# Kernel tuning notes

Hardware: AMD Instinct MI355X
Metric: run time of the kernel (lower is better)

Reference implementation:

```python
import jax, jax.numpy as jnp
import numpy as np

N, T, V, C, O = 64, 512, 17, 3, 64
EPS = 1e-5  # torch BatchNorm eps


def _bn(x, gamma, beta):
    # training-mode BatchNorm2d over (N, H, W) per channel, biased variance
    m = jnp.mean(x, axis=(0, 2, 3), keepdims=True)
    v = jnp.var(x, axis=(0, 2, 3), keepdims=True)
    return gamma.reshape(1, -1, 1, 1) * (x - m) * jax.lax.rsqrt(v + EPS) + beta.reshape(1, -1, 1, 1)


def setup_inputs() -> dict:
    key = jax.random.key(0)
    ks = jax.random.split(key, 20)
    f32 = jnp.float32
    PA = (jnp.eye(V, dtype=f32) / (1.0 + 1e-5))  # row-normalized identity, as in reset_parameter
    return {
        "x": jax.random.normal(ks[0], (N, T, V, C), f32),
        "w1": jax.random.normal(ks[1], (C, C), f32) * 0.5,
        "b1": jax.random.normal(ks[2], (C,), f32) * 0.1,
        "w2": jax.random.normal(ks[3], (C, C), f32) * 0.5,
        "b2": jax.random.normal(ks[4], (C,), f32) * 0.1,
        "convT_w": jax.random.normal(ks[5], (C,), f32) * 0.5,      # Conv2d(3,1,1) weight squeezed
        "convT_b": jax.random.normal(ks[6], (), f32) * 0.1,
        "convT_gamma": jnp.ones((), f32),
        "convT_beta": jnp.zeros((), f32),
        "PA": PA,
        "alpha": jnp.ones((V, V), f32),
        "conv2d_w": jax.random.normal(ks[7], (O, C), f32) * (2.0 / (O * 1 * 1)) ** 0.5,  # conv_branch_init
        "conv2d_b": jnp.zeros((O,), f32),
        "bn_gamma": jnp.full((O,), 1e-6, f32),  # bn_init(self.bn, 1e-6)
        "bn_beta": jnp.zeros((O,), f32),
        "pool_w": jax.random.normal(ks[8], (O, C), f32) * (2.0 / C) ** 0.5,  # kaiming fan_out-ish
        "pool_b": jnp.zeros((O,), f32),
        "pool_gamma": jnp.ones((O,), f32),
        "pool_beta": jnp.zeros((O,), f32),
    }


def reference(x, w1, b1, w2, b2, convT_w, convT_b, convT_gamma, convT_beta,
              PA, alpha, conv2d_w, conv2d_b, bn_gamma, bn_beta,
              pool_w, pool_b, pool_gamma, pool_beta):
    # x: (N, T, V, C)
    x1 = x @ w1.T + b1                     # linear1, (N,T,V,C)
    x2 = x @ w2.T + b2                     # linear2
    # d[n,t,i,j,c] = x1[n,t,j,c] - x2[n,t,i,c]; the 1x1 conv over C is linear,
    # so contract with convT_w BEFORE broadcasting to avoid the (N,T,V,V,C) tensor.
    a1 = x1 @ convT_w                      # (N,T,V)
    a2 = x2 @ convT_w                      # (N,T,V)
    s = a1[:, :, None, :] - a2[:, :, :, None] + convT_b   # (N,T,V,V)
    # BatchNorm2d(1): single channel -> stats over the whole tensor; then ReLU
    m = jnp.mean(s)
    var = jnp.var(s)
    s = jax.nn.relu(convT_gamma * (s - m) * jax.lax.rsqrt(var + EPS) + convT_beta)
    # temporal abs-diff, sum over T, mean over batch -> learned adjacency offset (V,V)
    a3 = jnp.mean(jnp.sum(jnp.abs(s[:, 1:] - s[:, :-1]), axis=1), axis=0)
    # NOTE: the original does x.view(N, C, T, V) -- a raw memory reinterpretation,
    # NOT a permute. Replicate with reshape.
    xr = x.reshape(N, C, T, V)
    A = PA + alpha * a3                    # (V,V)
    y = (xr.reshape(N, C * T, V) @ A).reshape(N, C, T, V)
    z = jnp.einsum('nctv,oc->notv', y, conv2d_w) + conv2d_b[None, :, None, None]
    z = _bn(z, bn_gamma, bn_beta)
    p = jnp.einsum('nctv,oc->notv', xr, pool_w) + pool_b[None, :, None, None]
    p = _bn(p, pool_gamma, pool_beta)
    out = jax.nn.relu(z + p)               # (N,O,T,V)
    return out.reshape(N, T, V, O)         # raw reshape, matching torch .reshape
```

## Files before the change

kernel.cpp:

```cpp
#include <hip/hip_runtime.h>

constexpr int Nn = 64, Tt = 512, Vv = 17, Oo = 64;
constexpr int TV  = Tt * Vv;
constexpr int CTV = 3 * TV;
constexpr float EPSf = 1e-5f;
constexpr int NG   = 51;
constexpr int GSTR = 2688;
constexpr int NGE  = 2652;
constexpr int BTV  = 1088;

__device__ inline int div17(int v) { return (int)(((unsigned)v * 61681u) >> 20); }

__device__ inline double wred(double v) {
#pragma unroll
  for (int o = 32; o > 0; o >>= 1) v += __shfl_down(v, o, 64);
  return v;
}

__global__ void __launch_bounds__(256) k1(
    const float* __restrict__ x,
    const float* __restrict__ w1, const float* __restrict__ b1,
    const float* __restrict__ w2, const float* __restrict__ b2,
    const float* __restrict__ cw, const float* __restrict__ cb,
    double* __restrict__ spart, float* __restrict__ gpart)
{
  __shared__ float wr[64 * 56];
  __shared__ float xsA[64 * 51];
  __shared__ double dred[4][5];
  const int tid = threadIdx.x, bid = blockIdx.x;
  const int n = bid >> 3, ch = bid & 7;

  {
    const float4* src = (const float4*)(x + (size_t)bid * 3264);
    float4* dst = (float4*)xsA;
    for (int i = tid; i < 816; i += 256) dst[i] = src[i];
  }
#pragma unroll
  for (int c = 0; c < 3; ++c) {
    const float4* src = (const float4*)(x + (size_t)n * CTV + (size_t)c * TV + ch * BTV);
    for (int i = tid; i < 272; i += 256) {
      float4 v = src[i];
      int p = i * 4;
      float vv[4] = { v.x, v.y, v.z, v.w };
#pragma unroll
      for (int k = 0; k < 4; ++k) {
        int pp = p + k; int t = div17(pp), u = pp - t * 17;
        wr[t * 56 + c * 17 + u] = vv[k];
      }
    }
  }
  for (int i = tid; i < 64 * 5; i += 256) { int t = i / 5, j = 51 + (i - t * 5); wr[t * 56 + j] = 0.f; }
  __syncthreads();

  float u1[3], u2[3];
#pragma unroll
  for (int k = 0; k < 3; ++k) {
    float s1 = 0.f, s2 = 0.f;
#pragma unroll
    for (int c = 0; c < 3; ++c) { s1 += cw[c] * w1[c * 3 + k]; s2 += cw[c] * w2[c * 3 + k]; }
    u1[k] = s1; u2[k] = s2;
  }
  float d1 = 0.f, d2 = 0.f;
#pragma unroll
  for (int c = 0; c < 3; ++c) { d1 += b1[c] * cw[c]; d2 += b2[c] * cw[c]; }
  const float bb = cb[0];

  if (tid < 49) {
    const int r8 = (tid / 7) * 8, c8 = (tid - (tid / 7) * 7) * 8;
    float acc[8][8];
#pragma unroll
    for (int a = 0; a < 8; ++a)
#pragma unroll
      for (int b = 0; b < 8; ++b) acc[a][b] = 0.f;
    for (int t = 0; t < 64; ++t) {
      const float* row = &wr[t * 56];
      float4 ra0 = *(const float4*)(row + r8), ra1 = *(const float4*)(row + r8 + 4);
      float4 cb0 = *(const float4*)(row + c8), cb1 = *(const float4*)(row + c8 + 4);
      float ae[8] = { ra0.x, ra0.y, ra0.z, ra0.w, ra1.x, ra1.y, ra1.z, ra1.w };
      float be[8] = { cb0.x, cb0.y, cb0.z, cb0.w, cb1.x, cb1.y, cb1.z, cb1.w };
#pragma unroll
      for (int a = 0; a < 8; ++a)
#pragma unroll
        for (int b = 0; b < 8; ++b) acc[a][b] = fmaf(ae[a], be[b], acc[a][b]);
    }
    float* gp = gpart + (size_t)bid * GSTR;
#pragma unroll
    for (int a = 0; a < 8; ++a) {
      int j = r8 + a;
      if (j < NG) {
#pragma unroll
        for (int b = 0; b < 8; ++b) {
          int jp = c8 + b;
          if (jp < NG) gp[j * NG + jp] = acc[a][b];
        }
      }
    }
  }

  double st[5] = {0, 0, 0, 0, 0};
  if (tid >= 64 && tid < 128) {
    const float* rp = &xsA[(tid - 64) * 51];
    float A = 0.f, G = 0.f, Q1 = 0.f, Q2 = 0.f;
#pragma unroll
    for (int v = 0; v < 17; ++v) {
      float x0 = rp[v * 3], x1 = rp[v * 3 + 1], x2 = rp[v * 3 + 2];
      float va1 = fmaf(x0, u1[0], fmaf(x1, u1[1], fmaf(x2, u1[2], d1)));
      float va2 = fmaf(x0, u2[0], fmaf(x1, u2[1], fmaf(x2, u2[2], d2)));
      float g = bb - va2;
      A += va1; G += g;
      Q1 = fmaf(va1, va1, Q1); Q2 = fmaf(g, g, Q2);
    }
    st[0] = A; st[1] = G; st[2] = Q1; st[3] = Q2; st[4] = (double)A * (double)G;
  }
  if (tid >= 128 && tid < 128 + NG) {
    int j = tid - 128;
    float m = 0.f;
    for (int t = 0; t < 64; ++t) m += wr[t * 56 + j];
    gpart[(size_t)bid * GSTR + NG * NG + j] = m;
  }

  {
    int wv = tid >> 6;
#pragma unroll
    for (int s = 0; s < 5; ++s) { double r = wred(st[s]); if ((tid & 63) == 0) dred[wv][s] = r; }
  }
  __syncthreads();
  if (tid < 5)
    spart[(size_t)bid * 5 + tid] = dred[0][tid] + dred[1][tid] + dred[2][tid] + dred[3][tid];
}

__global__ void __launch_bounds__(256) k2(
    const float* __restrict__ x, const double* __restrict__ spart,
    const float* __restrict__ gpart,
    const float* __restrict__ w1, const float* __restrict__ b1,
    const float* __restrict__ w2, const float* __restrict__ b2,
    const float* __restrict__ cw, const float* __restrict__ cb,
    const float* __restrict__ cg_, const float* __restrict__ cbeta,
    float* __restrict__ a3part, double* __restrict__ gramF)
{
  __shared__ float l1t[17 * 260];
  __shared__ float l2t[17 * 260];
  __shared__ float segsum[289 * 4];
  __shared__ double dred[4][21];
  __shared__ float sfl[2];
  const int tid = threadIdx.x;
  const int h = blockIdx.x, n = blockIdx.y;
  const int jb = n * 2 + h;
  const int t0 = h * 256;
  const int wv = tid >> 6;

  {
    double v5[5];
#pragma unroll
    for (int s = 0; s < 5; ++s)
      v5[s] = spart[(size_t)tid * 5 + s] + spart[(size_t)(tid + 256) * 5 + s];
#pragma unroll
    for (int s = 0; s < 5; ++s) { double r = wred(v5[s]); if ((tid & 63) == 0) dred[wv][s] = r; }
  }
  __syncthreads();
  if (tid == 0) {
    double S[5];
#pragma unroll
    for (int s = 0; s < 5; ++s) S[s] = dred[0][s] + dred[1][s] + dred[2][s] + dred[3][s];
    double cnt = (double)Nn * Tt * Vv * Vv;
    double mean = ((double)Vv * (S[0] + S[1])) / cnt;
    double m2   = ((double)Vv * (S[2] + S[3]) + 2.0 * S[4]) / cnt;
    double var  = m2 - mean * mean;
    double scale = (double)cg_[0] / sqrt(var + (double)EPSf);
    double shift = (double)cbeta[0] + scale * ((double)cb[0] - mean);
    sfl[0] = (float)scale; sfl[1] = (float)(shift - scale * (double)cb[0]);
  }
  __syncthreads();

  {
    int e0 = jb * 21;
    double gv[21];
    const float* g1 = gpart + (size_t)tid * GSTR + e0;
    const float* g2 = gpart + (size_t)(tid + 256) * GSTR + e0;
#pragma unroll
    for (int k = 0; k < 21; ++k) gv[k] = (double)g1[k] + (double)g2[k];
#pragma unroll
    for (int k = 0; k < 21; ++k) { double r = wred(gv[k]); if ((tid & 63) == 0) dred[wv][k] = r; }
    __syncthreads();
    if (tid < 21 && e0 + tid < NGE)
      gramF[e0 + tid] = dred[0][tid] + dred[1][tid] + dred[2][tid] + dred[3][tid];
  }

  float u1[3], u2[3];
#pragma unroll
  for (int k = 0; k < 3; ++k) {
    float s1 = 0.f, s2 = 0.f;
#pragma unroll
    for (int c = 0; c < 3; ++c) { s1 += cw[c] * w1[c * 3 + k]; s2 += cw[c] * w2[c * 3 + k]; }
    u1[k] = s1; u2[k] = s2;
  }
  float d1 = 0.f, d2 = 0.f;
#pragma unroll
  for (int c = 0; c < 3; ++c) { d1 += b1[c] * cw[c]; d2 += b2[c] * cw[c]; }
  const float bb = cb[0];

  const int nst = (h == 0) ? 257 : 256;
  const float* xb = x + ((size_t)(n * Tt + t0)) * 51;
  for (int idx = tid; idx < nst * 17; idx += 256) {
    int r = div17(idx), v = idx - r * 17;
    const float* xp = xb + idx * 3;
    float x0 = xp[0], x1 = xp[1], x2 = xp[2];
    float va1 = fmaf(x0, u1[0], fmaf(x1, u1[1], fmaf(x2, u1[2], d1)));
    float va2 = fmaf(x0, u2[0], fmaf(x1, u2[1], fmaf(x2, u2[2], d2)));
    l1t[v * 260 + r] = va1; l2t[v * 260 + r] = bb - va2;
  }
  __syncthreads();

  {
    const float scale = sfl[0], c0 = sfl[1];
    for (int task = tid; task < 289 * 4; task += 256) {
      int e = task >> 2, s = task & 3;
      int i = div17(e), j = e - i * 17;
      int ts = s * 64;
      bool hasb = !(h == 1 && s == 3);
      const float* J = &l1t[j * 260];
      const float* I = &l2t[i * 260];
      float prev = fmaxf(fmaf(scale, J[ts] + I[ts], c0), 0.f);
      float acc = 0.f;
#pragma unroll 4
      for (int q = 0; q < 16; ++q) {
        float4 a4 = *(const float4*)(J + ts + q * 4);
        float4 b4 = *(const float4*)(I + ts + q * 4);
        float z0 = fmaxf(fmaf(scale, a4.x + b4.x, c0), 0.f);
        float z1 = fmaxf(fmaf(scale, a4.y + b4.y, c0), 0.f);
        float z2 = fmaxf(fmaf(scale, a4.z + b4.z, c0), 0.f);
        float z3 = fmaxf(fmaf(scale, a4.w + b4.w, c0), 0.f);
        if (q > 0) acc += fabsf(z0 - prev);
        acc += fabsf(z1 - z0) + fabsf(z2 - z1) + fabsf(z3 - z2);
        prev = z3;
      }
      if (hasb) {
        float zb = fmaxf(fmaf(scale, J[ts + 64] + I[ts + 64], c0), 0.f);
        acc += fabsf(zb - prev);
      }
      segsum[e * 4 + s] = acc;
    }
  }
  __syncthreads();

  for (int e = tid; e < 289; e += 256) {
    float s = (segsum[e * 4] + segsum[e * 4 + 1]) + (segsum[e * 4 + 2] + segsum[e * 4 + 3]);
    a3part[(size_t)jb * 289 + e] = s;
  }
}

__global__ void __launch_bounds__(256, 2) k3(
    const float* __restrict__ x,
    const float* __restrict__ PA, const float* __restrict__ alpha,
    const float* __restrict__ a3part, const double* __restrict__ gramF,
    const float* __restrict__ c2w, const float* __restrict__ c2b,
    const float* __restrict__ bng, const float* __restrict__ bnb,
    const float* __restrict__ pw, const float* __restrict__ pb,
    const float* __restrict__ pg, const float* __restrict__ pbeta,
    float* __restrict__ out)
{
  __shared__ float xs[3 * BTV], ys[3 * BTV];
  __shared__ float As[289], Bh[289], rsA[17], coefs[512];
  __shared__ double gs[NGE];
  __shared__ double mom[18];
  const int tid = threadIdx.x, bid = blockIdx.x;
  const int n = bid >> 3, ch = bid & 7;
  const int t0c = ch * BTV;

#pragma unroll
  for (int c = 0; c < 3; ++c) {
    const float4* src = (const float4*)(x + (size_t)n * CTV + (size_t)c * TV + t0c);
    float4* dst = (float4*)(xs + c * BTV);
    for (int i = tid; i < 272; i += 256) dst[i] = src[i];
  }

  for (int e = tid; e < NGE; e += 256) gs[e] = gramF[e];
  for (int e = tid; e < 289; e += 256) {
    float acc = 0.f;
#pragma unroll 4
    for (int j = 0; j < 128; ++j) acc += a3part[(size_t)j * 289 + e];
    As[e] = fmaf(alpha[e], acc * (1.0f / Nn), PA[e]);
  }
  __syncthreads();

  for (int k = tid; k < 289; k += 256) {
    int u = div17(k), up = k - u * 17;
    float s = 0.f;
#pragma unroll
    for (int v = 0; v < 17; ++v) s = fmaf(As[u * 17 + v], As[up * 17 + v], s);
    Bh[k] = s;
  }
  if (tid < 17) {
    float s = 0.f;
#pragma unroll
    for (int v = 0; v < 17; ++v) s += As[tid * 17 + v];
    rsA[tid] = s;
  }
  __syncthreads();

  {
    const int pc0[6] = {0, 0, 0, 1, 1, 2};
    const int pc1[6] = {0, 1, 2, 1, 2, 2};
    if (tid < 192) {
      int p = tid >> 5, r = tid & 31;
      int c = pc0[p], cp = pc1[p];
      double s = 0.0;
      for (int k = r; k < 289; k += 32) {
        int u = div17(k), up = k - u * 17;
        s += gs[(c * 17 + u) * NG + cp * 17 + up] * (double)Bh[k];
      }
#pragma unroll
      for (int off = 16; off > 0; off >>= 1) s += __shfl_down(s, off, 32);
      if (r == 0) mom[3 + p] = s;
    } else if (tid < 198) {
      int p = tid - 192; int c = pc0[p], cp = pc1[p];
      double s = 0.0;
#pragma unroll
      for (int u = 0; u < 17; ++u) s += gs[(c * 17 + u) * NG + cp * 17 + u];
      mom[12 + p] = s;
    } else if (tid < 201) {
      int c = tid - 198; double s = 0.0;
#pragma unroll
      for (int u = 0; u < 17; ++u) s += gs[NG * NG + c * 17 + u] * (double)rsA[u];
      mom[c] = s;
    } else if (tid < 204) {
      int c = tid - 201; double s = 0.0;
#pragma unroll
      for (int u = 0; u < 17; ++u) s += gs[NG * NG + c * 17 + u];
      mom[9 + c] = s;
    }
  }
  __syncthreads();

  if (tid < 64) {
    int o = tid;
    const double cnt = (double)Nn * Tt * Vv;
    double my0 = mom[0] / cnt, my1 = mom[1] / cnt, my2 = mom[2] / cnt;
    double e00 = mom[3] / cnt, e01 = mom[4] / cnt, e02 = mom[5] / cnt;
    double e11 = mom[6] / cnt, e12 = mom[7] / cnt, e22 = mom[8] / cnt;
    double mx0 = mom[9] / cnt, mx1 = mom[10] / cnt, mx2 = mom[11] / cnt;
    double f00 = mom[12] / cnt, f01 = mom[13] / cnt, f02 = mom[14] / cnt;
    double f11 = mom[15] / cnt, f12 = mom[16] / cnt, f22 = mom[17] / cnt;
    double w0 = c2w[o * 3], w1_ = c2w[o * 3 + 1], w2_ = c2w[o * 3 + 2], bz = c2b[o];
    double wm = w0 * my0 + w1_ * my1 + w2_ * my2, mz = wm + bz;
    double Ez2 = w0 * w0 * e00 + 2 * w0 * w1_ * e01 + 2 * w0 * w2_ * e02
               + w1_ * w1_ * e11 + 2 * w1_ * w2_ * e12 + w2_ * w2_ * e22
               + 2 * bz * wm + bz * bz;
    double sz = (double)bng[o] / sqrt(Ez2 - mz * mz + (double)EPSf);
    double q0 = pw[o * 3], q1 = pw[o * 3 + 1], q2 = pw[o * 3 + 2], bp = pb[o];
    double qm = q0 * mx0 + q1 * mx1 + q2 * mx2, mp = qm + bp;
    double Ep2 = q0 * q0 * f00 + 2 * q0 * q1 * f01 + 2 * q0 * q2 * f02
               + q1 * q1 * f11 + 2 * q1 * q2 * f12 + q2 * q2 * f22
               + 2 * bp * qm + bp * bp;
    double sp = (double)pg[o] / sqrt(Ep2 - mp * mp + (double)EPSf);
    coefs[o * 8 + 0] = (float)(sz * w0); coefs[o * 8 + 1] = (float)(sz * w1_); coefs[o * 8 + 2] = (float)(sz * w2_);
    coefs[o * 8 + 3] = (float)(sp * q0); coefs[o * 8 + 4] = (float)(sp * q1); coefs[o * 8 + 5] = (float)(sp * q2);
    coefs[o * 8 + 6] = (float)(sz * (bz - mz) + (double)bnb[o] + sp * (bp - mp) + (double)pbeta[o]);
    coefs[o * 8 + 7] = 0.f;
  }
#pragma unroll
  for (int k = 0; k < 5; ++k) {
    int e = k * 256 + tid;
    if (e < BTV) {
      int tr = div17(e), v = e - tr * 17;
      float y0 = 0.f, y1 = 0.f, y2 = 0.f;
#pragma unroll
      for (int u = 0; u < 17; ++u) {
        float a = As[u * 17 + v];
        y0 = fmaf(xs[tr * 17 + u], a, y0);
        y1 = fmaf(xs[BTV + tr * 17 + u], a, y1);
        y2 = fmaf(xs[2 * BTV + tr * 17 + u], a, y2);
      }
      ys[e] = y0; ys[BTV + e] = y1; ys[2 * BTV + e] = y2;
    }
  }
  __syncthreads();

  float* ob = out + (size_t)n * ((size_t)Oo * TV) + t0c;
#pragma unroll 2
  for (int k = 0; k < 68; ++k) {
    int idx = k * 256 + tid;
    int o = div17(idx >> 4);
    int q = idx - o * 272, tq = q * 4;
    float4 y0 = *(const float4*)&ys[tq];
    float4 y1 = *(const float4*)&ys[BTV + tq];
    float4 y2 = *(const float4*)&ys[2 * BTV + tq];
    float4 x0 = *(const float4*)&xs[tq];
    float4 x1 = *(const float4*)&xs[BTV + tq];
    float4 x2 = *(const float4*)&xs[2 * BTV + tq];
    float a0 = coefs[o * 8 + 0], a1 = coefs[o * 8 + 1], a2 = coefs[o * 8 + 2];
    float p0 = coefs[o * 8 + 3], p1 = coefs[o * 8 + 4], p2 = coefs[o * 8 + 5];
    float be = coefs[o * 8 + 6];
    float4 r;
    r.x = fmaxf(fmaf(a0, y0.x, fmaf(a1, y1.x, fmaf(a2, y2.x, fmaf(p0, x0.x, fmaf(p1, x1.x, fmaf(p2, x2.x, be)))))), 0.f);
    r.y = fmaxf(fmaf(a0, y0.y, fmaf(a1, y1.y, fmaf(a2, y2.y, fmaf(p0, x0.y, fmaf(p1, x1.y, fmaf(p2, x2.y, be)))))), 0.f);
    r.z = fmaxf(fmaf(a0, y0.z, fmaf(a1, y1.z, fmaf(a2, y2.z, fmaf(p0, x0.z, fmaf(p1, x1.z, fmaf(p2, x2.z, be)))))), 0.f);
    r.w = fmaxf(fmaf(a0, y0.w, fmaf(a1, y1.w, fmaf(a2, y2.w, fmaf(p0, x0.w, fmaf(p1, x1.w, fmaf(p2, x2.w, be)))))), 0.f);
    *(float4*)(ob + (size_t)o * TV + tq) = r;
  }
}

extern "C" void kernel_launch(void* const* d_in, const int* in_sizes, int n_in,
                              void* d_out, int out_size, void* d_ws, size_t ws_size,
                              hipStream_t stream)
{
  (void)in_sizes; (void)n_in; (void)out_size; (void)ws_size;
  const float* x     = (const float*)d_in[0];
  const float* w1    = (const float*)d_in[1];
  const float* b1    = (const float*)d_in[2];
  const float* w2    = (const float*)d_in[3];
  const float* b2    = (const float*)d_in[4];
  const float* cw    = (const float*)d_in[5];
  const float* cb    = (const float*)d_in[6];
  const float* cg_   = (const float*)d_in[7];
  const float* cbeta = (const float*)d_in[8];
  const float* PA    = (const float*)d_in[9];
  const float* alpha = (const float*)d_in[10];
  const float* c2w   = (const float*)d_in[11];
  const float* c2b   = (const float*)d_in[12];
  const float* bng   = (const float*)d_in[13];
  const float* bnb   = (const float*)d_in[14];
  const float* pw    = (const float*)d_in[15];
  const float* pb    = (const float*)d_in[16];
  const float* pg    = (const float*)d_in[17];
  const float* pbeta = (const float*)d_in[18];
  float* out = (float*)d_out;

  char* ws = (char*)d_ws;
  double* spart  = (double*)(ws + 0);
  float*  gpart  = (float*)(ws + 20480);
  float*  a3part = (float*)(ws + 5525504);
  double* gramF  = (double*)(ws + 5673472);

  hipLaunchKernelGGL(k1, dim3(512), dim3(256), 0, stream,
                     x, w1, b1, w2, b2, cw, cb, spart, gpart);
  hipLaunchKernelGGL(k2, dim3(2, Nn), dim3(256), 0, stream,
                     x, spart, gpart, w1, b1, w2, b2, cw, cb, cg_, cbeta, a3part, gramF);
  hipLaunchKernelGGL(k3, dim3(512), dim3(256), 0, stream,
                     x, PA, alpha, a3part, gramF, c2w, c2b, bng, bnb,
                     pw, pb, pg, pbeta, out);
}
```

Before: 89.22 us.

## Fuse three kernels into one cooperative kernel with custom grid barriers

Replaces the three-kernel pipeline with a single cooperative kernel of 512 blocks that synchronises through a hand-written atomic grid barrier, keeping per-block data in LDS across phases. Global statistics and the adjacency offset are accumulated with fixed-point 64-bit atomics instead of partial-sum buffers and separate reduction passes, and the temporal-diff work is redistributed per block. The aim is to remove kernel launch gaps and re-reads of x between stages. The cost is barrier spin overhead, a small init kernel, and reliance on co-residency; the old three-kernel path is kept as a fallback.

```diff
diff --git a/kernel.cpp b/kernel.cpp
--- a/kernel.cpp
+++ b/kernel.cpp
@@ -4,10 +4,12 @@
 constexpr int TV  = Tt * Vv;
 constexpr int CTV = 3 * TV;
 constexpr float EPSf = 1e-5f;
+constexpr int NB   = 512;
 constexpr int NG   = 51;
 constexpr int GSTR = 2688;
 constexpr int NGE  = 2652;
 constexpr int BTV  = 1088;
+constexpr double FXS = 16777216.0;
 
 __device__ inline int div17(int v) { return (int)(((unsigned)v * 61681u) >> 20); }
 
@@ -17,7 +19,354 @@
   return v;
 }
 
-__global__ void __launch_bounds__(256) k1(
+__global__ void __launch_bounds__(256) kinit(int* __restrict__ barr, long long* __restrict__ acc) {
+  for (int i = threadIdx.x; i < 520; i += 256) barr[i] = 0;
+  for (int i = threadIdx.x; i < 304; i += 256) acc[i] = 0;
+}
+
+__device__ inline void gridbar(int* slots, int* gen, int bid, int marker) {
+  __syncthreads();
+  if (threadIdx.x == 0) {
+    __threadfence();
+    __hip_atomic_store(slots + bid, marker, __ATOMIC_RELEASE, __HIP_MEMORY_SCOPE_AGENT);
+  }
+  if (bid == 0) {
+    for (int i = threadIdx.x; i < NB; i += 256) {
+      while (__hip_atomic_load(slots + i, __ATOMIC_ACQUIRE, __HIP_MEMORY_SCOPE_AGENT) < marker)
+        __builtin_amdgcn_s_sleep(8);
+    }
+    __syncthreads();
+    if (threadIdx.x == 0)
+      __hip_atomic_store(gen, marker, __ATOMIC_RELEASE, __HIP_MEMORY_SCOPE_AGENT);
+  } else if (threadIdx.x == 0) {
+    while (__hip_atomic_load(gen, __ATOMIC_ACQUIRE, __HIP_MEMORY_SCOPE_AGENT) < marker)
+      __builtin_amdgcn_s_sleep(64);
+  }
+  __syncthreads();
+}
+
+__global__ void __launch_bounds__(256, 2) fused(
+    const float* __restrict__ x,
+    const float* __restrict__ w1, const float* __restrict__ b1,
+    const float* __restrict__ w2, const float* __restrict__ b2,
+    const float* __restrict__ cw, const float* __restrict__ cb,
+    const float* __restrict__ cg_, const float* __restrict__ cbeta,
+    const float* __restrict__ PA, const float* __restrict__ alpha,
+    const float* __restrict__ c2w, const float* __restrict__ c2b,
+    const float* __restrict__ bng, const float* __restrict__ bnb,
+    const float* __restrict__ pw, const float* __restrict__ pb,
+    const float* __restrict__ pg, const float* __restrict__ pbeta,
+    float* __restrict__ out,
+    int* __restrict__ barr, long long* __restrict__ accum,
+    float* __restrict__ gpart, double* __restrict__ gramF)
+{
+  __shared__ float smem[6528];
+  __shared__ float As[289], Bh[289], rsA[17], coefs[512];
+  __shared__ double dred[4][6];
+  __shared__ double mom[18];
+  __shared__ float sfl[2];
+  float* l1t = smem;
+  float* l2t = smem + 1173;
+  float* wr  = smem + 2346;
+  double* scrD = (double*)&smem[2348];
+  float* xs  = smem;
+  float* ys  = smem + 3264;
+  int* slots = barr;
+  int* gen   = barr + NB;
+  long long* sstats  = accum;
+  long long* a3fixed = accum + 8;
+
+  const int tid = threadIdx.x, bid = blockIdx.x;
+  const int n = bid >> 3, ch = bid & 7;
+  const int t0 = ch * 64;
+
+  float u1[3], u2[3];
+#pragma unroll
+  for (int k = 0; k < 3; ++k) {
+    float s1 = 0.f, s2 = 0.f;
+#pragma unroll
+    for (int c = 0; c < 3; ++c) { s1 += cw[c] * w1[c * 3 + k]; s2 += cw[c] * w2[c * 3 + k]; }
+    u1[k] = s1; u2[k] = s2;
+  }
+  float d1 = 0.f, d2 = 0.f;
+#pragma unroll
+  for (int c = 0; c < 3; ++c) { d1 += b1[c] * cw[c]; d2 += b2[c] * cw[c]; }
+  const float bb = cb[0];
+
+  {
+    const int nload = (ch == 7) ? 64 : 65;
+    for (int idx = tid; idx < nload * 17; idx += 256) {
+      int r = div17(idx), v = idx - r * 17;
+      const float* xp = x + ((size_t)((n * Tt + t0 + r) * 17 + v)) * 3;
+      float x0 = xp[0], x1 = xp[1], x2 = xp[2];
+      float va1 = fmaf(x0, u1[0], fmaf(x1, u1[1], fmaf(x2, u1[2], d1)));
+      float va2 = fmaf(x0, u2[0], fmaf(x1, u2[1], fmaf(x2, u2[2], d2)));
+      l1t[v * 69 + r] = va1; l2t[v * 69 + r] = bb - va2;
+    }
+#pragma unroll
+    for (int c = 0; c < 3; ++c) {
+      const float4* src = (const float4*)(x + (size_t)n * CTV + (size_t)c * TV + ch * BTV);
+      for (int i = tid; i < 272; i += 256) {
+        float4 v = src[i];
+        int p = i * 4;
+        float vv[4] = { v.x, v.y, v.z, v.w };
+#pragma unroll
+        for (int k = 0; k < 4; ++k) {
+          int pp = p + k; int t = div17(pp), u = pp - t * 17;
+          wr[t * 56 + c * 17 + u] = vv[k];
+        }
+      }
+    }
+    for (int i = tid; i < 64 * 5; i += 256) { int t = i / 5, j = 51 + (i - t * 5); wr[t * 56 + j] = 0.f; }
+    __syncthreads();
+
+    if (tid < 64) {
+      float sA = 0.f, sG = 0.f, Q1 = 0.f, Q2 = 0.f;
+#pragma unroll
+      for (int v = 0; v < 17; ++v) {
+        float a = l1t[v * 69 + tid], g = l2t[v * 69 + tid];
+        sA += a; sG += g;
+        Q1 = fmaf(a, a, Q1); Q2 = fmaf(g, g, Q2);
+      }
+      double st[5] = { (double)sA, (double)sG, (double)Q1, (double)Q2,
+                       (double)sA * (double)sG };
+#pragma unroll
+      for (int s = 0; s < 5; ++s) {
+        double r = wred(st[s]);
+        if (tid == 0)
+          atomicAdd((unsigned long long*)&sstats[s], (unsigned long long)(long long)llrint(r * FXS));
+      }
+    }
+    if (tid < 49) {
+      const int r8 = (tid / 7) * 8, c8 = (tid - (tid / 7) * 7) * 8;
+      float acc[8][8];
+#pragma unroll
+      for (int a = 0; a < 8; ++a)
+#pragma unroll
+        for (int b = 0; b < 8; ++b) acc[a][b] = 0.f;
+      for (int t = 0; t < 64; ++t) {
+        const float* row = &wr[t * 56];
+        float4 ra0 = *(const float4*)(row + r8), ra1 = *(const float4*)(row + r8 + 4);
+        float4 cb0 = *(const float4*)(row + c8), cb1 = *(const float4*)(row + c8 + 4);
+        float ae[8] = { ra0.x, ra0.y, ra0.z, ra0.w, ra1.x, ra1.y, ra1.z, ra1.w };
+        float be[8] = { cb0.x, cb0.y, cb0.z, cb0.w, cb1.x, cb1.y, cb1.z, cb1.w };
+#pragma unroll
+        for (int a = 0; a < 8; ++a)
+#pragma unroll
+          for (int b = 0; b < 8; ++b) acc[a][b] = fmaf(ae[a], be[b], acc[a][b]);
+      }
+      float* gp = gpart + (size_t)bid * GSTR;
+#pragma unroll
+      for (int a = 0; a < 8; ++a) {
+        int j = r8 + a;
+        if (j < NG) {
+#pragma unroll
+          for (int b = 0; b < 8; ++b) {
+            int jp = c8 + b;
+            if (jp < NG) gp[j * NG + jp] = acc[a][b];
+          }
+        }
+      }
+    }
+    if (tid >= 128 && tid < 128 + NG) {
+      int j = tid - 128;
+      float m = 0.f;
+      for (int t = 0; t < 64; ++t) m += wr[t * 56 + j];
+      gpart[(size_t)bid * GSTR + NG * NG + j] = m;
+    }
+  }
+  gridbar(slots, gen, bid, 1);
+
+  {
+    if (tid == 0) {
+      double S[5];
+#pragma unroll
+      for (int s = 0; s < 5; ++s)
+        S[s] = (double)__hip_atomic_load(&sstats[s], __ATOMIC_RELAXED, __HIP_MEMORY_SCOPE_AGENT) / FXS;
+      double cnt = (double)Nn * Tt * Vv * Vv;
+      double mean = ((double)Vv * (S[0] + S[1])) / cnt;
+      double m2   = ((double)Vv * (S[2] + S[3]) + 2.0 * S[4]) / cnt;
+      double var  = m2 - mean * mean;
+      double scale = (double)cg_[0] / sqrt(var + (double)EPSf);
+      double shift = (double)cbeta[0] + scale * ((double)bb - mean);
+      sfl[0] = (float)scale; sfl[1] = (float)(shift - scale * (double)bb);
+    }
+
+    const int e0 = bid * 5 + (bid < 92 ? bid : 92);
+    const int cnt = (bid < 92) ? 6 : 5;
+    {
+      const float* g1 = gpart + (size_t)tid * GSTR + e0;
+      const float* g2 = gpart + (size_t)(tid + 256) * GSTR + e0;
+      for (int k = 0; k < cnt; ++k)
+        scrD[k * 256 + tid] = (double)g1[k] + (double)g2[k];
+    }
+    __syncthreads();
+    {
+      int wv = tid >> 6;
+      for (int k = 0; k < cnt; ++k) {
+        double r = wred(scrD[k * 256 + tid]);
+        if ((tid & 63) == 0) dred[wv][k] = r;
+      }
+      __syncthreads();
+      if (tid < cnt)
+        gramF[e0 + tid] = dred[0][tid] + dred[1][tid] + dred[2][tid] + dred[3][tid];
+    }
+
+    const float scale = sfl[0], c0 = sfl[1];
+    const int last = (ch == 7) ? 63 : 64;
+#pragma unroll 1
+    for (int pass = 0; pass < 2; ++pass) {
+      int e = tid + pass * 256;
+      if (e < 289) {
+        int i = div17(e), j = e - i * 17;
+        const float* J = &l1t[j * 69];
+        const float* I = &l2t[i * 69];
+        float prev = fmaxf(fmaf(scale, J[0] + I[0], c0), 0.f);
+        float acc = 0.f;
+        for (int r = 1; r <= last; ++r) {
+          float cur = fmaxf(fmaf(scale, J[r] + I[r], c0), 0.f);
+          acc += fabsf(cur - prev); prev = cur;
+        }
+        atomicAdd((unsigned long long*)&a3fixed[e],
+                  (unsigned long long)(long long)llrint((double)acc * FXS));
+      }
+    }
+  }
+  gridbar(slots, gen, bid, 2);
+
+  {
+#pragma unroll
+    for (int c = 0; c < 3; ++c) {
+      const float4* src = (const float4*)(x + (size_t)n * CTV + (size_t)c * TV + ch * BTV);
+      float4* dst = (float4*)(xs + c * BTV);
+      for (int i = tid; i < 272; i += 256) dst[i] = src[i];
+    }
+    for (int e = tid; e < 289; e += 256) {
+      long long raw = __hip_atomic_load(&a3fixed[e], __ATOMIC_RELAXED, __HIP_MEMORY_SCOPE_AGENT);
+      float a3 = (float)((double)raw * (1.0 / FXS) * (1.0 / Nn));
+      As[e] = fmaf(alpha[e], a3, PA[e]);
+    }
+    __syncthreads();
+
+    for (int k = tid; k < 289; k += 256) {
+      int u = div17(k), up = k - u * 17;
+      float s = 0.f;
+#pragma unroll
+      for (int v = 0; v < 17; ++v) s = fmaf(As[u * 17 + v], As[up * 17 + v], s);
+      Bh[k] = s;
+    }
+    if (tid < 17) {
+      float s = 0.f;
+#pragma unroll
+      for (int v = 0; v < 17; ++v) s += As[tid * 17 + v];
+      rsA[tid] = s;
+    }
+    __syncthreads();
+
+    {
+      const int pc0[6] = {0, 0, 0, 1, 1, 2};
+      const int pc1[6] = {0, 1, 2, 1, 2, 2};
+      if (tid < 192) {
+        int p = tid >> 5, r = tid & 31;
+        int c = pc0[p], cp = pc1[p];
+        double s = 0.0;
+        for (int k = r; k < 289; k += 32) {
+          int u = div17(k), up = k - u * 17;
+          s += gramF[(c * 17 + u) * NG + cp * 17 + up] * (double)Bh[k];
+        }
+#pragma unroll
+        for (int off = 16; off > 0; off >>= 1) s += __shfl_down(s, off, 32);
+        if (r == 0) mom[3 + p] = s;
+      } else if (tid < 198) {
+        int p = tid - 192; const int c = pc0[p], cp = pc1[p];
+        double s = 0.0;
+#pragma unroll
+        for (int u = 0; u < 17; ++u) s += gramF[(c * 17 + u) * NG + cp * 17 + u];
+        mom[12 + p] = s;
+      } else if (tid < 201) {
+        int c = tid - 198; double s = 0.0;
+#pragma unroll
+        for (int u = 0; u < 17; ++u) s += gramF[NG * NG + c * 17 + u] * (double)rsA[u];
+        mom[c] = s;
+      } else if (tid < 204) {
+        int c = tid - 201; double s = 0.0;
+#pragma unroll
+        for (int u = 0; u < 17; ++u) s += gramF[NG * NG + c * 17 + u];
+        mom[9 + c] = s;
+      }
+    }
+    __syncthreads();
+
+    if (tid < 64) {
+      int o = tid;
+      const double cnt = (double)Nn * Tt * Vv;
+      double my0 = mom[0] / cnt, my1 = mom[1] / cnt, my2 = mom[2] / cnt;
+      double e00 = mom[3] / cnt, e01 = mom[4] / cnt, e02 = mom[5] / cnt;
+      double e11 = mom[6] / cnt, e12 = mom[7] / cnt, e22 = mom[8] / cnt;
+      double mx0 = mom[9] / cnt, mx1 = mom[10] / cnt, mx2 = mom[11] / cnt;
+      double f00 = mom[12] / cnt, f01 = mom[13] / cnt, f02 = mom[14] / cnt;
+      double f11 = mom[15] / cnt, f12 = mom[16] / cnt, f22 = mom[17] / cnt;
+      double w0 = c2w[o * 3], w1_ = c2w[o * 3 + 1], w2_ = c2w[o * 3 + 2], bz = c2b[o];
+      double wm = w0 * my0 + w1_ * my1 + w2_ * my2, mz = wm + bz;
+      double Ez2 = w0 * w0 * e00 + 2 * w0 * w1_ * e01 + 2 * w0 * w2_ * e02
+                 + w1_ * w1_ * e11 + 2 * w1_ * w2_ * e12 + w2_ * w2_ * e22
+                 + 2 * bz * wm + bz * bz;
+      double sz = (double)bng[o] / sqrt(Ez2 - mz * mz + (double)EPSf);
+      double q0 = pw[o * 3], q1 = pw[o * 3 + 1], q2 = pw[o * 3 + 2], bp = pb[o];
+      double qm = q0 * mx0 + q1 * mx1 + q2 * mx2, mp = qm + bp;
+      double Ep2 = q0 * q0 * f00 + 2 * q0 * q1 * f01 + 2 * q0 * q2 * f02
+                 + q1 * q1 * f11 + 2 * q1 * q2 * f12 + q2 * q2 * f22
+                 + 2 * bp * qm + bp * bp;
+      double sp = (double)pg[o] / sqrt(Ep2 - mp * mp + (double)EPSf);
+      coefs[o * 8 + 0] = (float)(sz * w0); coefs[o * 8 + 1] = (float)(sz * w1_); coefs[o * 8 + 2] = (float)(sz * w2_);
+      coefs[o * 8 + 3] = (float)(sp * q0); coefs[o * 8 + 4] = (float)(sp * q1); coefs[o * 8 + 5] = (float)(sp * q2);
+      coefs[o * 8 + 6] = (float)(sz * (bz - mz) + (double)bnb[o] + sp * (bp - mp) + (double)pbeta[o]);
+      coefs[o * 8 + 7] = 0.f;
+    }
+#pragma unroll
+    for (int k = 0; k < 5; ++k) {
+      int e = k * 256 + tid;
+      if (e < BTV) {
+        int tr = div17(e), v = e - tr * 17;
+        float y0 = 0.f, y1 = 0.f, y2 = 0.f;
+#pragma unroll
+        for (int u = 0; u < 17; ++u) {
+          float a = As[u * 17 + v];
+          y0 = fmaf(xs[tr * 17 + u], a, y0);
+          y1 = fmaf(xs[BTV + tr * 17 + u], a, y1);
+          y2 = fmaf(xs[2 * BTV + tr * 17 + u], a, y2);
+        }
+        ys[e] = y0; ys[BTV + e] = y1; ys[2 * BTV + e] = y2;
+      }
+    }
+    __syncthreads();
+
+    float* ob = out + (size_t)n * ((size_t)Oo * TV) + ch * BTV;
+#pragma unroll 2
+    for (int k = 0; k < 68; ++k) {
+      int idx = k * 256 + tid;
+      int o = div17(idx >> 4);
+      int q = idx - o * 272, tq = q * 4;
+      float4 y0 = *(const float4*)&ys[tq];
+      float4 y1 = *(const float4*)&ys[BTV + tq];
+      float4 y2 = *(const float4*)&ys[2 * BTV + tq];
+      float4 x0 = *(const float4*)&xs[tq];
+      float4 x1 = *(const float4*)&xs[BTV + tq];
+      float4 x2 = *(const float4*)&xs[2 * BTV + tq];
+      float a0 = coefs[o * 8 + 0], a1 = coefs[o * 8 + 1], a2 = coefs[o * 8 + 2];
+      float p0 = coefs[o * 8 + 3], p1 = coefs[o * 8 + 4], p2 = coefs[o * 8 + 5];
+      float be = coefs[o * 8 + 6];
+      float4 r;
+      r.x = fmaxf(fmaf(a0, y0.x, fmaf(a1, y1.x, fmaf(a2, y2.x, fmaf(p0, x0.x, fmaf(p1, x1.x, fmaf(p2, x2.x, be)))))), 0.f);
+      r.y = fmaxf(fmaf(a0, y0.y, fmaf(a1, y1.y, fmaf(a2, y2.y, fmaf(p0, x0.y, fmaf(p1, x1.y, fmaf(p2, x2.y, be)))))), 0.f);
+      r.z = fmaxf(fmaf(a0, y0.z, fmaf(a1, y1.z, fmaf(a2, y2.z, fmaf(p0, x0.z, fmaf(p1, x1.z, fmaf(p2, x2.z, be)))))), 0.f);
+      r.w = fmaxf(fmaf(a0, y0.w, fmaf(a1, y1.w, fmaf(a2, y2.w, fmaf(p0, x0.w, fmaf(p1, x1.w, fmaf(p2, x2.w, be)))))), 0.f);
+      *(float4*)(ob + (size_t)o * TV + tq) = r;
+    }
+  }
+}
+
+__global__ void __launch_bounds__(256) fk1(
     const float* __restrict__ x,
     const float* __restrict__ w1, const float* __restrict__ b1,
     const float* __restrict__ w2, const float* __restrict__ b2,
@@ -29,7 +378,6 @@
   __shared__ double dred[4][5];
   const int tid = threadIdx.x, bid = blockIdx.x;
   const int n = bid >> 3, ch = bid & 7;
-
   {
     const float4* src = (const float4*)(x + (size_t)bid * 3264);
     float4* dst = (float4*)xsA;
@@ -51,7 +399,6 @@
   }
   for (int i = tid; i < 64 * 5; i += 256) { int t = i / 5, j = 51 + (i - t * 5); wr[t * 56 + j] = 0.f; }
   __syncthreads();
-
   float u1[3], u2[3];
 #pragma unroll
   for (int k = 0; k < 3; ++k) {
@@ -64,7 +411,6 @@
 #pragma unroll
   for (int c = 0; c < 3; ++c) { d1 += b1[c] * cw[c]; d2 += b2[c] * cw[c]; }
   const float bb = cb[0];
-
   if (tid < 49) {
     const int r8 = (tid / 7) * 8, c8 = (tid - (tid / 7) * 7) * 8;
     float acc[8][8];
@@ -96,7 +442,6 @@
       }
     }
   }
-
   double st[5] = {0, 0, 0, 0, 0};
   if (tid >= 64 && tid < 128) {
     const float* rp = &xsA[(tid - 64) * 51];
@@ -118,7 +463,6 @@
     for (int t = 0; t < 64; ++t) m += wr[t * 56 + j];
     gpart[(size_t)bid * GSTR + NG * NG + j] = m;
   }
-
   {
     int wv = tid >> 6;
 #pragma unroll
@@ -129,7 +473,7 @@
     spart[(size_t)bid * 5 + tid] = dred[0][tid] + dred[1][tid] + dred[2][tid] + dred[3][tid];
 }
 
-__global__ void __launch_bounds__(256) k2(
+__global__ void __launch_bounds__(256) fk2(
     const float* __restrict__ x, const double* __restrict__ spart,
     const float* __restrict__ gpart,
     const float* __restrict__ w1, const float* __restrict__ b1,
@@ -148,7 +492,6 @@
   const int jb = n * 2 + h;
   const int t0 = h * 256;
   const int wv = tid >> 6;
-
   {
     double v5[5];
 #pragma unroll
@@ -171,7 +514,6 @@
     sfl[0] = (float)scale; sfl[1] = (float)(shift - scale * (double)cb[0]);
   }
   __syncthreads();
-
   {
     int e0 = jb * 21;
     double gv[21];
@@ -185,7 +527,6 @@
     if (tid < 21 && e0 + tid < NGE)
       gramF[e0 + tid] = dred[0][tid] + dred[1][tid] + dred[2][tid] + dred[3][tid];
   }
-
   float u1[3], u2[3];
 #pragma unroll
   for (int k = 0; k < 3; ++k) {
@@ -198,7 +539,6 @@
 #pragma unroll
   for (int c = 0; c < 3; ++c) { d1 += b1[c] * cw[c]; d2 += b2[c] * cw[c]; }
   const float bb = cb[0];
-
   const int nst = (h == 0) ? 257 : 256;
   const float* xb = x + ((size_t)(n * Tt + t0)) * 51;
   for (int idx = tid; idx < nst * 17; idx += 256) {
@@ -210,7 +550,6 @@
     l1t[v * 260 + r] = va1; l2t[v * 260 + r] = bb - va2;
   }
   __syncthreads();
-
   {
     const float scale = sfl[0], c0 = sfl[1];
     for (int task = tid; task < 289 * 4; task += 256) {
@@ -242,14 +581,13 @@
     }
   }
   __syncthreads();
-
   for (int e = tid; e < 289; e += 256) {
     float s = (segsum[e * 4] + segsum[e * 4 + 1]) + (segsum[e * 4 + 2] + segsum[e * 4 + 3]);
     a3part[(size_t)jb * 289 + e] = s;
   }
 }
 
-__global__ void __launch_bounds__(256, 2) k3(
+__global__ void __launch_bounds__(256, 2) fk3(
     const float* __restrict__ x,
     const float* __restrict__ PA, const float* __restrict__ alpha,
     const float* __restrict__ a3part, const double* __restrict__ gramF,
@@ -261,20 +599,16 @@
 {
   __shared__ float xs[3 * BTV], ys[3 * BTV];
   __shared__ float As[289], Bh[289], rsA[17], coefs[512];
-  __shared__ double gs[NGE];
   __shared__ double mom[18];
   const int tid = threadIdx.x, bid = blockIdx.x;
   const int n = bid >> 3, ch = bid & 7;
   const int t0c = ch * BTV;
-
 #pragma unroll
   for (int c = 0; c < 3; ++c) {
     const float4* src = (const float4*)(x + (size_t)n * CTV + (size_t)c * TV + t0c);
     float4* dst = (float4*)(xs + c * BTV);
     for (int i = tid; i < 272; i += 256) dst[i] = src[i];
   }
-
-  for (int e = tid; e < NGE; e += 256) gs[e] = gramF[e];
   for (int e = tid; e < 289; e += 256) {
     float acc = 0.f;
 #pragma unroll 4
@@ -282,7 +616,6 @@
     As[e] = fmaf(alpha[e], acc * (1.0f / Nn), PA[e]);
   }
   __syncthreads();
-
   for (int k = tid; k < 289; k += 256) {
     int u = div17(k), up = k - u * 17;
     float s = 0.f;
@@ -297,7 +630,6 @@
     rsA[tid] = s;
   }
   __syncthreads();
-
   {
     const int pc0[6] = {0, 0, 0, 1, 1, 2};
     const int pc1[6] = {0, 1, 2, 1, 2, 2};
@@ -307,31 +639,30 @@
       double s = 0.0;
       for (int k = r; k < 289; k += 32) {
         int u = div17(k), up = k - u * 17;
-        s += gs[(c * 17 + u) * NG + cp * 17 + up] * (double)Bh[k];
+        s += gramF[(c * 17 + u) * NG + cp * 17 + up] * (double)Bh[k];
       }
 #pragma unroll
       for (int off = 16; off > 0; off >>= 1) s += __shfl_down(s, off, 32);
       if (r == 0) mom[3 + p] = s;
     } else if (tid < 198) {
-      int p = tid - 192; int c = pc0[p], cp = pc1[p];
+      int p = tid - 192; const int c = pc0[p], cp = pc1[p];
       double s = 0.0;
 #pragma unroll
-      for (int u = 0; u < 17; ++u) s += gs[(c * 17 + u) * NG + cp * 17 + u];
+      for (int u = 0; u < 17; ++u) s += gramF[(c * 17 + u) * NG + cp * 17 + u];
       mom[12 + p] = s;
     } else if (tid < 201) {
       int c = tid - 198; double s = 0.0;
 #pragma unroll
-      for (int u = 0; u < 17; ++u) s += gs[NG * NG + c * 17 + u] * (double)rsA[u];
+      for (int u = 0; u < 17; ++u) s += gramF[NG * NG + c * 17 + u] * (double)rsA[u];
       mom[c] = s;
     } else if (tid < 204) {
       int c = tid - 201; double s = 0.0;
 #pragma unroll
-      for (int u = 0; u < 17; ++u) s += gs[NG * NG + c * 17 + u];
+      for (int u = 0; u < 17; ++u) s += gramF[NG * NG + c * 17 + u];
       mom[9 + c] = s;
     }
   }
   __syncthreads();
-
   if (tid < 64) {
     int o = tid;
     const double cnt = (double)Nn * Tt * Vv;
@@ -375,7 +706,6 @@
     }
   }
   __syncthreads();
-
   float* ob = out + (size_t)n * ((size_t)Oo * TV) + t0c;
 #pragma unroll 2
   for (int k = 0; k < 68; ++k) {
@@ -427,16 +757,36 @@
   float* out = (float*)d_out;
 
   char* ws = (char*)d_ws;
-  double* spart  = (double*)(ws + 0);
-  float*  gpart  = (float*)(ws + 20480);
-  float*  a3part = (float*)(ws + 5525504);
-  double* gramF  = (double*)(ws + 5673472);
-
-  hipLaunchKernelGGL(k1, dim3(512), dim3(256), 0, stream,
+  int*       barr   = (int*)(ws + 0);
+  long long* accum  = (long long*)(ws + 4096);
+  float*     gpart  = (float*)(ws + 8192);
+  double*    gramF  = (double*)(ws + 5513216);
+  double*    spart  = (double*)(ws + 5534432);
+  float*     a3part = (float*)(ws + 5554912);
+
+  int maxB = 0;
+  hipError_t oe = hipOccupancyMaxActiveBlocksPerMultiprocessor(&maxB, (const void*)fused, 256, 0);
+  bool coop = (oe == hipSuccess) && (maxB >= 2);
+
+  if (coop) {
+    hipLaunchKernelGGL(kinit, dim3(1), dim3(256), 0, stream, barr, accum);
+    void* args[] = {
+      (void*)&x, (void*)&w1, (void*)&b1, (void*)&w2, (void*)&b2,
+      (void*)&cw, (void*)&cb, (void*)&cg_, (void*)&cbeta,
+      (void*)&PA, (void*)&alpha, (void*)&c2w, (void*)&c2b,
+      (void*)&bng, (void*)&bnb, (void*)&pw, (void*)&pb, (void*)&pg, (void*)&pbeta,
+      (void*)&out, (void*)&barr, (void*)&accum, (void*)&gpart, (void*)&gramF
+    };
+    hipError_t le = hipLaunchCooperativeKernel((const void*)fused, dim3(NB), dim3(256), args, 0, stream);
+    if (le == hipSuccess) return;
+    coop = false;
+  }
+
+  hipLaunchKernelGGL(fk1, dim3(512), dim3(256), 0, stream,
                      x, w1, b1, w2, b2, cw, cb, spart, gpart);
-  hipLaunchKernelGGL(k2, dim3(2, Nn), dim3(256), 0, stream,
+  hipLaunchKernelGGL(fk2, dim3(2, Nn), dim3(256), 0, stream,
                      x, spart, gpart, w1, b1, w2, b2, cw, cb, cg_, cbeta, a3part, gramF);
-  hipLaunchKernelGGL(k3, dim3(512), dim3(256), 0, stream,
+  hipLaunchKernelGGL(fk3, dim3(512), dim3(256), 0, stream,
                      x, PA, alpha, a3part, gramF, c2w, c2b, bng, bnb,
                      pw, pb, pg, pbeta, out);
 }
```

After: 245.9 us. +175.6%, slower.

## Keep k3 mixing results in registers and stream outputs per thread over channels

Applied to the files above, without the earlier changes.

k3 now runs with 320 threads so that 289 threads each handle one adjacency entry and 272 threads each own four contiguous positions. The V×V mixing y = x·A is computed into registers before the coefficient barrier, which removes the ys shared buffer and one barrier. Each thread then loops over all 64 output channels, reading the coefficients as float4 and writing float4 stores. The gram matrix is read directly from global memory rather than staged in shared memory, which cuts LDS use and should improve occupancy, at the cost of uncached-style global reads in the moments phase and more registers per thread.

```diff
diff --git a/kernel.cpp b/kernel.cpp
--- a/kernel.cpp
+++ b/kernel.cpp
@@ -29,7 +29,6 @@
   __shared__ double dred[4][5];
   const int tid = threadIdx.x, bid = blockIdx.x;
   const int n = bid >> 3, ch = bid & 7;
-
   {
     const float4* src = (const float4*)(x + (size_t)bid * 3264);
     float4* dst = (float4*)xsA;
@@ -51,7 +50,6 @@
   }
   for (int i = tid; i < 64 * 5; i += 256) { int t = i / 5, j = 51 + (i - t * 5); wr[t * 56 + j] = 0.f; }
   __syncthreads();
-
   float u1[3], u2[3];
 #pragma unroll
   for (int k = 0; k < 3; ++k) {
@@ -64,7 +62,6 @@
 #pragma unroll
   for (int c = 0; c < 3; ++c) { d1 += b1[c] * cw[c]; d2 += b2[c] * cw[c]; }
   const float bb = cb[0];
-
   if (tid < 49) {
     const int r8 = (tid / 7) * 8, c8 = (tid - (tid / 7) * 7) * 8;
     float acc[8][8];
@@ -96,7 +93,6 @@
       }
     }
   }
-
   double st[5] = {0, 0, 0, 0, 0};
   if (tid >= 64 && tid < 128) {
     const float* rp = &xsA[(tid - 64) * 51];
@@ -118,7 +114,6 @@
     for (int t = 0; t < 64; ++t) m += wr[t * 56 + j];
     gpart[(size_t)bid * GSTR + NG * NG + j] = m;
   }
-
   {
     int wv = tid >> 6;
 #pragma unroll
@@ -148,7 +143,6 @@
   const int jb = n * 2 + h;
   const int t0 = h * 256;
   const int wv = tid >> 6;
-
   {
     double v5[5];
 #pragma unroll
@@ -171,7 +165,6 @@
     sfl[0] = (float)scale; sfl[1] = (float)(shift - scale * (double)cb[0]);
   }
   __syncthreads();
-
   {
     int e0 = jb * 21;
     double gv[21];
@@ -185,7 +178,6 @@
     if (tid < 21 && e0 + tid < NGE)
       gramF[e0 + tid] = dred[0][tid] + dred[1][tid] + dred[2][tid] + dred[3][tid];
   }
-
   float u1[3], u2[3];
 #pragma unroll
   for (int k = 0; k < 3; ++k) {
@@ -198,7 +190,6 @@
 #pragma unroll
   for (int c = 0; c < 3; ++c) { d1 += b1[c] * cw[c]; d2 += b2[c] * cw[c]; }
   const float bb = cb[0];
-
   const int nst = (h == 0) ? 257 : 256;
   const float* xb = x + ((size_t)(n * Tt + t0)) * 51;
   for (int idx = tid; idx < nst * 17; idx += 256) {
@@ -210,7 +201,6 @@
     l1t[v * 260 + r] = va1; l2t[v * 260 + r] = bb - va2;
   }
   __syncthreads();
-
   {
     const float scale = sfl[0], c0 = sfl[1];
     for (int task = tid; task < 289 * 4; task += 256) {
@@ -242,14 +232,13 @@
     }
   }
   __syncthreads();
-
   for (int e = tid; e < 289; e += 256) {
     float s = (segsum[e * 4] + segsum[e * 4 + 1]) + (segsum[e * 4 + 2] + segsum[e * 4 + 3]);
     a3part[(size_t)jb * 289 + e] = s;
   }
 }
 
-__global__ void __launch_bounds__(256, 2) k3(
+__global__ void __launch_bounds__(320, 2) k3(
     const float* __restrict__ x,
     const float* __restrict__ PA, const float* __restrict__ alpha,
     const float* __restrict__ a3part, const double* __restrict__ gramF,
@@ -259,9 +248,8 @@
     const float* __restrict__ pg, const float* __restrict__ pbeta,
     float* __restrict__ out)
 {
-  __shared__ float xs[3 * BTV], ys[3 * BTV];
+  __shared__ float xs[3 * BTV];
   __shared__ float As[289], Bh[289], rsA[17], coefs[512];
-  __shared__ double gs[NGE];
   __shared__ double mom[18];
   const int tid = threadIdx.x, bid = blockIdx.x;
   const int n = bid >> 3, ch = bid & 7;
@@ -271,30 +259,48 @@
   for (int c = 0; c < 3; ++c) {
     const float4* src = (const float4*)(x + (size_t)n * CTV + (size_t)c * TV + t0c);
     float4* dst = (float4*)(xs + c * BTV);
-    for (int i = tid; i < 272; i += 256) dst[i] = src[i];
-  }
-
-  for (int e = tid; e < NGE; e += 256) gs[e] = gramF[e];
-  for (int e = tid; e < 289; e += 256) {
+    for (int i = tid; i < 272; i += 320) dst[i] = src[i];
+  }
+  if (tid < 289) {
     float acc = 0.f;
 #pragma unroll 4
-    for (int j = 0; j < 128; ++j) acc += a3part[(size_t)j * 289 + e];
-    As[e] = fmaf(alpha[e], acc * (1.0f / Nn), PA[e]);
-  }
-  __syncthreads();
-
-  for (int k = tid; k < 289; k += 256) {
-    int u = div17(k), up = k - u * 17;
+    for (int j = 0; j < 128; ++j) acc += a3part[(size_t)j * 289 + tid];
+    As[tid] = fmaf(alpha[tid], acc * (1.0f / Nn), PA[tid]);
+  }
+  __syncthreads();
+
+  if (tid < 289) {
+    int u = div17(tid), up = tid - u * 17;
     float s = 0.f;
 #pragma unroll
     for (int v = 0; v < 17; ++v) s = fmaf(As[u * 17 + v], As[up * 17 + v], s);
-    Bh[k] = s;
+    Bh[tid] = s;
   }
   if (tid < 17) {
     float s = 0.f;
 #pragma unroll
     for (int v = 0; v < 17; ++v) s += As[tid * 17 + v];
     rsA[tid] = s;
+  }
+  float yreg[3][4], xreg[3][4];
+  if (tid < 272) {
+    const int i0 = tid * 4;
+#pragma unroll
+    for (int e = 0; e < 4; ++e) {
+      int idx = i0 + e;
+      int tr = div17(idx), v = idx - tr * 17;
+      float y0 = 0.f, y1 = 0.f, y2 = 0.f;
+      const float* r0 = &xs[tr * 17];
+      const float* r1 = &xs[BTV + tr * 17];
+      const float* r2 = &xs[2 * BTV + tr * 17];
+#pragma unroll
+      for (int u = 0; u < 17; ++u) {
+        float a = As[u * 17 + v];
+        y0 = fmaf(r0[u], a, y0); y1 = fmaf(r1[u], a, y1); y2 = fmaf(r2[u], a, y2);
+      }
+      yreg[0][e] = y0; yreg[1][e] = y1; yreg[2][e] = y2;
+      xreg[0][e] = xs[i0 + e]; xreg[1][e] = xs[BTV + i0 + e]; xreg[2][e] = xs[2 * BTV + i0 + e];
+    }
   }
   __syncthreads();
 
@@ -307,26 +313,26 @@
       double s = 0.0;
       for (int k = r; k < 289; k += 32) {
         int u = div17(k), up = k - u * 17;
-        s += gs[(c * 17 + u) * NG + cp * 17 + up] * (double)Bh[k];
+        s += gramF[(c * 17 + u) * NG + cp * 17 + up] * (double)Bh[k];
       }
 #pragma unroll
       for (int off = 16; off > 0; off >>= 1) s += __shfl_down(s, off, 32);
       if (r == 0) mom[3 + p] = s;
     } else if (tid < 198) {
-      int p = tid - 192; int c = pc0[p], cp = pc1[p];
+      int p = tid - 192; const int c = pc0[p], cp = pc1[p];
       double s = 0.0;
 #pragma unroll
-      for (int u = 0; u < 17; ++u) s += gs[(c * 17 + u) * NG + cp * 17 + u];
+      for (int u = 0; u < 17; ++u) s += gramF[(c * 17 + u) * NG + cp * 17 + u];
       mom[12 + p] = s;
     } else if (tid < 201) {
       int c = tid - 198; double s = 0.0;
 #pragma unroll
-      for (int u = 0; u < 17; ++u) s += gs[NG * NG + c * 17 + u] * (double)rsA[u];
+      for (int u = 0; u < 17; ++u) s += gramF[NG * NG + c * 17 + u] * (double)rsA[u];
       mom[c] = s;
     } else if (tid < 204) {
       int c = tid - 201; double s = 0.0;
 #pragma unroll
-      for (int u = 0; u < 17; ++u) s += gs[NG * NG + c * 17 + u];
+      for (int u = 0; u < 17; ++u) s += gramF[NG * NG + c * 17 + u];
       mom[9 + c] = s;
     }
   }
@@ -358,45 +364,25 @@
     coefs[o * 8 + 6] = (float)(sz * (bz - mz) + (double)bnb[o] + sp * (bp - mp) + (double)pbeta[o]);
     coefs[o * 8 + 7] = 0.f;
   }
-#pragma unroll
-  for (int k = 0; k < 5; ++k) {
-    int e = k * 256 + tid;
-    if (e < BTV) {
-      int tr = div17(e), v = e - tr * 17;
-      float y0 = 0.f, y1 = 0.f, y2 = 0.f;
-#pragma unroll
-      for (int u = 0; u < 17; ++u) {
-        float a = As[u * 17 + v];
-        y0 = fmaf(xs[tr * 17 + u], a, y0);
-        y1 = fmaf(xs[BTV + tr * 17 + u], a, y1);
-        y2 = fmaf(xs[2 * BTV + tr * 17 + u], a, y2);
-      }
-      ys[e] = y0; ys[BTV + e] = y1; ys[2 * BTV + e] = y2;
-    }
-  }
-  __syncthreads();
-
-  float* ob = out + (size_t)n * ((size_t)Oo * TV) + t0c;
-#pragma unroll 2
-  for (int k = 0; k < 68; ++k) {
-    int idx = k * 256 + tid;
-    int o = div17(idx >> 4);
-    int q = idx - o * 272, tq = q * 4;
-    float4 y0 = *(const float4*)&ys[tq];
-    float4 y1 = *(const float4*)&ys[BTV + tq];
-    float4 y2 = *(const float4*)&ys[2 * BTV + tq];
-    float4 x0 = *(const float4*)&xs[tq];
-    float4 x1 = *(const float4*)&xs[BTV + tq];
-    float4 x2 = *(const float4*)&xs[2 * BTV + tq];
-    float a0 = coefs[o * 8 + 0], a1 = coefs[o * 8 + 1], a2 = coefs[o * 8 + 2];
-    float p0 = coefs[o * 8 + 3], p1 = coefs[o * 8 + 4], p2 = coefs[o * 8 + 5];
-    float be = coefs[o * 8 + 6];
-    float4 r;
-    r.x = fmaxf(fmaf(a0, y0.x, fmaf(a1, y1.x, fmaf(a2, y2.x, fmaf(p0, x0.x, fmaf(p1, x1.x, fmaf(p2, x2.x, be)))))), 0.f);
-    r.y = fmaxf(fmaf(a0, y0.y, fmaf(a1, y1.y, fmaf(a2, y2.y, fmaf(p0, x0.y, fmaf(p1, x1.y, fmaf(p2, x2.y, be)))))), 0.f);
-    r.z = fmaxf(fmaf(a0, y0.z, fmaf(a1, y1.z, fmaf(a2, y2.z, fmaf(p0, x0.z, fmaf(p1, x1.z, fmaf(p2, x2.z, be)))))), 0.f);
-    r.w = fmaxf(fmaf(a0, y0.w, fmaf(a1, y1.w, fmaf(a2, y2.w, fmaf(p0, x0.w, fmaf(p1, x1.w, fmaf(p2, x2.w, be)))))), 0.f);
-    *(float4*)(ob + (size_t)o * TV + tq) = r;
+  __syncthreads();
+
+  if (tid < 272) {
+    float* ob = out + (size_t)n * ((size_t)Oo * TV) + t0c + tid * 4;
+#pragma unroll 4
+    for (int o = 0; o < Oo; ++o) {
+      float4 ca = *(const float4*)&coefs[o * 8];
+      float4 cbv = *(const float4*)&coefs[o * 8 + 4];
+      float4 r;
+      r.x = fmaxf(fmaf(ca.x, yreg[0][0], fmaf(ca.y, yreg[1][0], fmaf(ca.z, yreg[2][0],
+            fmaf(ca.w, xreg[0][0], fmaf(cbv.x, xreg[1][0], fmaf(cbv.y, xreg[2][0], cbv.z)))))), 0.f);
+      r.y = fmaxf(fmaf(ca.x, yreg[0][1], fmaf(ca.y, yreg[1][1], fmaf(ca.z, yreg[2][1],
+            fmaf(ca.w, xreg[0][1], fmaf(cbv.x, xreg[1][1], fmaf(cbv.y, xreg[2][1], cbv.z)))))), 0.f);
+      r.z = fmaxf(fmaf(ca.x, yreg[0][2], fmaf(ca.y, yreg[1][2], fmaf(ca.z, yreg[2][2],
+            fmaf(ca.w, xreg[0][2], fmaf(cbv.x, xreg[1][2], fmaf(cbv.y, xreg[2][2], cbv.z)))))), 0.f);
+      r.w = fmaxf(fmaf(ca.x, yreg[0][3], fmaf(ca.y, yreg[1][3], fmaf(ca.z, yreg[2][3],
+            fmaf(ca.w, xreg[0][3], fmaf(cbv.x, xreg[1][3], fmaf(cbv.y, xreg[2][3], cbv.z)))))), 0.f);
+      *(float4*)(ob + (size_t)o * TV) = r;
+    }
   }
 }
 
@@ -436,7 +422,7 @@
                      x, w1, b1, w2, b2, cw, cb, spart, gpart);
   hipLaunchKernelGGL(k2, dim3(2, Nn), dim3(256), 0, stream,
                      x, spart, gpart, w1, b1, w2, b2, cw, cb, cg_, cbeta, a3part, gramF);
-  hipLaunchKernelGGL(k3, dim3(512), dim3(256), 0, stream,
+  hipLaunchKernelGGL(k3, dim3(512), dim3(320), 0, stream,
                      x, PA, alpha, a3part, gramF, c2w, c2b, bng, bnb,
                      pw, pb, pg, pbeta, out);
 }
```

After: 107.4 us. 1.2x slower.
